# Optimization experiments

Measured on AMD Instinct MI355X. Metric: run time of the kernel, lower is better.

Reference implementation:

```python
import jax, jax.numpy as jnp
import numpy as np

P = 16      # patch size
DM = 512    # d_model
DI = 1024   # d_inner = expand * d_model
N = 16      # d_state
K = 4       # d_conv
DR = 32     # dt_rank = ceil(d_model/16)
NL = 8      # n_layers
NC = 1000   # num_classes


def _ln(x, w, b):
    m = x.mean(-1, keepdims=True)
    v = x.var(-1, keepdims=True)
    return (x - m) * jax.lax.rsqrt(v + 1e-5) * w + b


def _fpad(x, wl, wr, ht, hb):
    # torch F.pad(x, (wl, wr, ht, hb)) with possibly negative (crop) values, NCHW
    x = jnp.pad(x, ((0, 0), (0, 0), (max(ht, 0), max(hb, 0)), (max(wl, 0), max(wr, 0))))
    return x[:, :, -min(ht, 0):x.shape[2] + min(hb, 0), -min(wl, 0):x.shape[3] + min(wr, 0)]


def _mamba(x, in_w, conv_w, conv_b, xproj_w, dt_w, dt_b, A_log, Dp, out_w):
    # standard mamba_ssm Mamba layer; weights stored (in, out)
    B, L, _ = x.shape
    xz = x @ in_w                         # (B, L, 2*DI)
    xpart, z = xz[..., :DI], xz[..., DI:]
    # depthwise causal conv1d, kernel K, padding K-1 then truncate to L
    xc = jnp.pad(xpart.transpose(0, 2, 1), ((0, 0), (0, 0), (K - 1, 0)))  # (B, DI, L+K-1)
    conv = conv_b[None, :, None] + sum(conv_w[None, :, k, None] * xc[:, :, k:k + L] for k in range(K))
    u = jax.nn.silu(conv).transpose(0, 2, 1)    # (B, L, DI)
    dbc = u @ xproj_w                           # (B, L, DR + 2N)
    dt = jax.nn.softplus(dbc[..., :DR] @ dt_w + dt_b)  # (B, L, DI)
    Bm, Cm = dbc[..., DR:DR + N], dbc[..., DR + N:]
    A = -jnp.exp(A_log)                         # (DI, N)
    dA = jnp.exp(dt[..., None] * A)             # (B, L, DI, N)
    dBu = (dt * u)[..., None] * Bm[:, :, None, :]

    def step(h, inp):
        dA_t, dBu_t, C_t = inp
        h = dA_t * h + dBu_t                    # (B, DI, N)
        return h, jnp.einsum('bdn,bn->bd', h, C_t)

    h0 = jnp.zeros((B, DI, N), x.dtype)
    _, ys = jax.lax.scan(step, h0, (dA.transpose(1, 0, 2, 3), dBu.transpose(1, 0, 2, 3), Cm.transpose(1, 0, 2)))
    y = ys.transpose(1, 0, 2) + u * Dp          # (B, L, DI)
    return (y * jax.nn.silu(z)) @ out_w         # (B, L, DM)


def reference(img, patch_ln_w, patch_ln_b, patch_w, patch_b, pos_emb, cls_tok,
              ln_w, ln_b, in_w, conv_w, conv_b, xproj_w, dt_w, dt_b, A_log, D, out_w,
              head_ln_w, head_ln_b, head_w, head_b):
    shifts = ((1, -1, 0, 0), (-1, 1, 0, 0), (0, 0, 1, -1), (0, 0, -1, 1))
    x5 = jnp.concatenate([img] + [_fpad(img, *s) for s in shifts], axis=1)  # (B, 15, H, W)
    Bn, C, H, W = x5.shape
    # 'b c (h p1) (w p2) -> b (h w) (p1 p2 c)'
    x = x5.reshape(Bn, C, H // P, P, W // P, P).transpose(0, 2, 4, 3, 5, 1).reshape(Bn, (H // P) * (W // P), P * P * C)
    x = _ln(x, patch_ln_w, patch_ln_b) @ patch_w + patch_b  # (B, n, DM)
    n = x.shape[1]
    x = jnp.concatenate([x, jnp.broadcast_to(cls_tok, (Bn, 1, DM))], axis=1)  # cls appended at END
    x = x + pos_emb[:, :n + 1]
    for i in range(NL):
        y = _ln(x, ln_w[i], ln_b[i])
        x = x + _mamba(y, in_w[i], conv_w[i], conv_b[i], xproj_w[i], dt_w[i], dt_b[i], A_log[i], D[i], out_w[i])
    x = x[:, -1]  # pool='cls' -> last token
    return _ln(x, head_ln_w, head_ln_b) @ head_w + head_b


def setup_inputs() -> dict:
    key = jax.random.key(0)
    ks = jax.random.split(key, 12)
    B = 8
    PD = P * P * 15  # 3840
    rn = lambda k, shape, scale=1.0: jax.random.normal(k, shape, jnp.float32) * scale
    return {
        "img": rn(ks[0], (B, 3, 224, 224)),
        "patch_ln_w": jnp.ones((PD,), jnp.float32), "patch_ln_b": jnp.zeros((PD,), jnp.float32),
        "patch_w": rn(ks[1], (PD, DM), PD ** -0.5), "patch_b": jnp.zeros((DM,), jnp.float32),
        "pos_emb": rn(ks[2], (1, 197, DM), 0.02),
        "cls_tok": rn(ks[3], (1, 1, DM), 0.02),
        "ln_w": jnp.ones((NL, DM), jnp.float32), "ln_b": jnp.zeros((NL, DM), jnp.float32),
        "in_w": rn(ks[4], (NL, DM, 2 * DI), DM ** -0.5),
        "conv_w": rn(ks[5], (NL, DI, K), K ** -0.5),
        "conv_b": jnp.zeros((NL, DI), jnp.float32),
        "xproj_w": rn(ks[6], (NL, DI, DR + 2 * N), DI ** -0.5),
        "dt_w": rn(ks[7], (NL, DR, DI), DR ** -0.5),
        "dt_b": rn(ks[8], (NL, DI), 0.1) - 4.0,  # softplus -> small positive dt
        "A_log": jnp.log(jnp.broadcast_to(jnp.arange(1.0, N + 1.0, dtype=jnp.float32), (NL, DI, N))),
        "D": jnp.ones((NL, DI), jnp.float32),
        "out_w": rn(ks[9], (NL, DI, DM), DI ** -0.5),
        "head_ln_w": jnp.ones((DM,), jnp.float32), "head_ln_b": jnp.zeros((DM,), jnp.float32),
        "head_w": rn(ks[10], (DM, NC), DM ** -0.5), "head_b": jnp.zeros((NC,), jnp.float32),
    }
```

## Files before the change

kernel.cpp:

```cpp
#include <hip/hip_runtime.h>
#include <hip/hip_fp16.h>
#include <math.h>

#define BATCH   8
#define LSEQ    197
#define LPAD    200
#define NPATCH  196
#define NPTOK   (BATCH * NPATCH)
#define NTOK    (BATCH * LSEQ)
#define MPAD    1664
#define DMODEL  512
#define DINNER  1024
#define NSTATE  16
#define DRANK   32
#define NLAYER  8
#define NCLS    1000
#define PDIM    3840

typedef _Float16 f16x8 __attribute__((ext_vector_type(8)));
typedef float    f32x4 __attribute__((ext_vector_type(4)));
typedef unsigned short us8 __attribute__((ext_vector_type(8)));

__device__ __forceinline__ float f_rcp(float x) { return __builtin_amdgcn_rcpf(x); }
__device__ __forceinline__ float sp_silu(float x) { return x * f_rcp(1.0f + __expf(-x)); }
__device__ __forceinline__ float sp_softplus(float x) {
    return x > 20.0f ? x : __logf(1.0f + __expf(x));
}

#define DPP_ROW_SHR_STEP(P, NB, CTRL)                                          \
    {                                                                          \
        float t_[NB];                                                          \
        _Pragma("unroll")                                                      \
        for (int i_ = 0; i_ < NB; ++i_)                                        \
            t_[i_] = __int_as_float(__builtin_amdgcn_update_dpp(               \
                0, __float_as_int(P[i_]), CTRL, 0xF, 0xF, true));              \
        _Pragma("unroll")                                                      \
        for (int i_ = 0; i_ < NB; ++i_) P[i_] += t_[i_];                       \
    }

template <int NB>
__device__ __forceinline__ void row_sum16v(float* p) {
    DPP_ROW_SHR_STEP(p, NB, 0x111);
    DPP_ROW_SHR_STEP(p, NB, 0x112);
    DPP_ROW_SHR_STEP(p, NB, 0x114);
    DPP_ROW_SHR_STEP(p, NB, 0x118);
}

__device__ __forceinline__ void store_f16(char* __restrict__ Hb,
                                          int row, int k, int K, float v) {
    size_t byte = (size_t)row * (size_t)(K * 2) +
                  (size_t)(((unsigned)(k * 2)) ^ (unsigned)((row & 7) << 4));
    *(__half*)(Hb + byte) = __float2half_rn(v);
}

__device__ __forceinline__ void store_f16x4(char* __restrict__ Hb,
                                            int row, int k4, int K, float4 v) {
    size_t byte = (size_t)row * (size_t)(K * 2) +
                  (size_t)(((unsigned)(k4 * 2)) ^ (unsigned)((row & 7) << 4));
    *(ushort4*)(Hb + byte) = make_ushort4(
        __half_as_ushort(__float2half_rn(v.x)), __half_as_ushort(__float2half_rn(v.y)),
        __half_as_ushort(__float2half_rn(v.z)), __half_as_ushort(__float2half_rn(v.w)));
}

__device__ __forceinline__ float2 block_reduce2(float a, float b, float* lds) {
#pragma unroll
    for (int off = 32; off > 0; off >>= 1) {
        a += __shfl_down(a, off);
        b += __shfl_down(b, off);
    }
    int lane = threadIdx.x & 63, w = threadIdx.x >> 6;
    if (lane == 0) { lds[w] = a; lds[4 + w] = b; }
    __syncthreads();
    float sa = lds[0] + lds[1] + lds[2] + lds[3];
    float sb = lds[4] + lds[5] + lds[6] + lds[7];
    return make_float2(sa, sb);
}

__global__ __launch_bounds__(256) void k_patch_ln(
    const float* __restrict__ img, const float* __restrict__ lnw,
    const float* __restrict__ lnb, char* __restrict__ Xph) {
    __shared__ float vals[PDIM];
    __shared__ float red[8];
    int tok = blockIdx.x;
    int b = tok / NPATCH, p = tok % NPATCH;
    int gy = p / 14, gx = p % 14;
    int tid = threadIdx.x;
    int py = tid >> 4, px = tid & 15;
    int h0 = gy * 16 + py, w0 = gx * 16 + px;
    const int dh[5] = {0, 0, 0, -1, 1};
    const int dw[5] = {0, -1, 1, 0, 0};
    float s = 0.f, ss = 0.f;
#pragma unroll
    for (int c = 0; c < 15; ++c) {
        int g = c / 3, ch = c % 3;
        int h = h0 + dh[g], w = w0 + dw[g];
        float v = 0.f;
        if ((unsigned)h < 224u && (unsigned)w < 224u)
            v = img[((b * 3 + ch) * 224 + h) * 224 + w];
        vals[tid * 15 + c] = v;
        s += v; ss += v * v;
    }
    float2 t2 = block_reduce2(s, ss, red);
    float mean = t2.x * (1.0f / PDIM);
    float var  = t2.y * (1.0f / PDIM) - mean * mean;
    float rstd = 1.0f / sqrtf(var + 1e-5f);
    for (int j = 0; j < 15; ++j) {
        int e = tid + j * 256;
        float v = (vals[e] - mean) * rstd * lnw[e] + lnb[e];
        store_f16(Xph, tok, e, PDIM, v);
    }
}

__global__ __launch_bounds__(256) void k_ln(
    const float* __restrict__ x, const float* __restrict__ w,
    const float* __restrict__ b, char* __restrict__ yh) {
    __shared__ float red[8];
    int t = blockIdx.x, tid = threadIdx.x;
    const float* xr = x + (size_t)t * DMODEL;
    float v0 = xr[tid], v1 = xr[tid + 256];
    float2 t2 = block_reduce2(v0 + v1, v0 * v0 + v1 * v1, red);
    float mean = t2.x * (1.0f / DMODEL);
    float var  = t2.y * (1.0f / DMODEL) - mean * mean;
    float rstd = 1.0f / sqrtf(var + 1e-5f);
    store_f16(yh, t, tid,       DMODEL, (v0 - mean) * rstd * w[tid]       + b[tid]);
    store_f16(yh, t, tid + 256, DMODEL, (v1 - mean) * rstd * w[tid + 256] + b[tid + 256]);
}

__global__ __launch_bounds__(256) void k_red_ln(
    const float* __restrict__ part, float* __restrict__ xtok,
    const float* __restrict__ w, const float* __restrict__ b,
    char* __restrict__ yh) {
    __shared__ float red[8];
    int t = blockIdx.x, tid = threadIdx.x;
    size_t base = (size_t)t * DMODEL;
    float v0 = xtok[base + tid], v1 = xtok[base + tid + 256];
#pragma unroll
    for (int k = 0; k < 4; ++k) {
        v0 += part[(size_t)k * (NTOK * DMODEL) + base + tid];
        v1 += part[(size_t)k * (NTOK * DMODEL) + base + tid + 256];
    }
    xtok[base + tid] = v0;
    xtok[base + tid + 256] = v1;
    float2 t2 = block_reduce2(v0 + v1, v0 * v0 + v1 * v1, red);
    float mean = t2.x * (1.0f / DMODEL);
    float var  = t2.y * (1.0f / DMODEL) - mean * mean;
    float rstd = 1.0f / sqrtf(var + 1e-5f);
    store_f16(yh, t, tid,       DMODEL, (v0 - mean) * rstd * w[tid]       + b[tid]);
    store_f16(yh, t, tid + 256, DMODEL, (v1 - mean) * rstd * w[tid + 256] + b[tid + 256]);
}

__global__ __launch_bounds__(256) void k_wT(
    const float* __restrict__ W, char* __restrict__ Th,
    int Ks, int Ns, size_t wStride, size_t tByteStride) {
    __shared__ float t[32][33];
    int z = blockIdx.z;
    const float* Wz = W + (size_t)z * wStride;
    char* ThZ = Th + (size_t)z * tByteStride;
    int n0 = blockIdx.x * 32, k0 = blockIdx.y * 32;
    int tx = threadIdx.x, ty = threadIdx.y;
#pragma unroll
    for (int r = 0; r < 4; ++r) {
        int k = k0 + ty + r * 8, n = n0 + tx;
        t[tx][ty + r * 8] = (n < Ns) ? Wz[(size_t)k * Ns + n] : 0.f;
    }
    __syncthreads();
#pragma unroll
    for (int r = 0; r < 4; ++r) {
        int n = n0 + ty + r * 8, k = k0 + tx;
        float v = t[ty + r * 8][tx];
        size_t byte = (size_t)n * (size_t)(Ks * 2) +
                      (size_t)(((unsigned)(k * 2)) ^ (unsigned)((n & 7) << 4));
        *(__half*)(ThZ + byte) = __float2half_rn(v);
    }
}

template <bool F16OUT>
__global__ __launch_bounds__(256, 2) void k_gemm_f16(
    const char* __restrict__ Ah, const char* __restrict__ Bh,
    float* __restrict__ C, unsigned short* __restrict__ C16,
    int M, int N, int K, int kchunk, long partStride) {
    __shared__ __half L[2][2][128 * 64];
    const int tid = threadIdx.x, w = tid >> 6, lane = tid & 63;

    const int GX = gridDim.x, GY = gridDim.y;
    const int nwg = GX * GY * gridDim.z;
    const int orig = blockIdx.x + GX * (blockIdx.y + GY * blockIdx.z);
    const int q = nwg >> 3, r = nwg & 7, xcd = orig & 7, pos = orig >> 3;
    const int wrk = (xcd < r ? xcd * (q + 1) : r * (q + 1) + (xcd - r) * q) + pos;
    const int bm = wrk % GY;
    const int t1 = wrk / GY;
    const int bn = t1 % GX, bz = t1 / GX;

    const int m0 = bm * 128, n0 = bn * 128;
    const int kbeg = bz * kchunk;
    int kend = kbeg + kchunk; if (kend > K) kend = K;
    C += (size_t)bz * (size_t)partStride;
    const size_t K2 = (size_t)K * 2;
    const int srowBase = 32 * w;
    const int srLane = lane >> 3;
    const int scol = (lane & 7) * 16;

    f32x4 acc[4][4];
#pragma unroll
    for (int i = 0; i < 4; ++i)
#pragma unroll
        for (int j = 0; j < 4; ++j) acc[i][j] = (f32x4)(0.f);

    auto STAGE = [&](int buf, int k0) {
#pragma unroll
        for (int t = 0; t < 4; ++t) {
            int lr = srowBase + 8 * t;
            size_t ao = (size_t)(m0 + lr + srLane) * K2 + (size_t)k0 * 2 + scol;
            size_t bo = (size_t)(n0 + lr + srLane) * K2 + (size_t)k0 * 2 + scol;
            __builtin_amdgcn_global_load_lds(
                (const __attribute__((address_space(1))) void*)(Ah + ao),
                (__attribute__((address_space(3))) void*)&L[buf][0][lr * 64], 16, 0, 0);
            __builtin_amdgcn_global_load_lds(
                (const __attribute__((address_space(1))) void*)(Bh + bo),
                (__attribute__((address_space(3))) void*)&L[buf][1][lr * 64], 16, 0, 0);
        }
    };

    const int wr = (w >> 1) * 64, wc = (w & 1) * 64;
    const int g = lane >> 4, rr = lane & 15;
    const int nk = (kend - kbeg + 63) / 64;

    STAGE(0, kbeg);

    for (int t = 0; t < nk; ++t) {
        int cur = t & 1;
        if (t + 1 < nk) {
            STAGE(cur ^ 1, kbeg + (t + 1) * 64);
            asm volatile("s_waitcnt vmcnt(8)" ::: "memory");
        } else {
            asm volatile("s_waitcnt vmcnt(0)" ::: "memory");
        }
        __builtin_amdgcn_s_barrier();
        const __half* LA = L[cur][0];
        const __half* LB = L[cur][1];
#pragma unroll
        for (int kk = 0; kk < 2; ++kk) {
            f16x8 af[4], bf[4];
#pragma unroll
            for (int mf = 0; mf < 4; ++mf) {
                int row = wr + mf * 16 + rr;
                int off = row * 128 + ((kk * 64 + g * 16) ^ ((row & 7) << 4));
                af[mf] = *(const f16x8*)((const char*)LA + off);
            }
#pragma unroll
            for (int nf = 0; nf < 4; ++nf) {
                int row = wc + nf * 16 + rr;
                int off = row * 128 + ((kk * 64 + g * 16) ^ ((row & 7) << 4));
                bf[nf] = *(const f16x8*)((const char*)LB + off);
            }
#pragma unroll
            for (int mf = 0; mf < 4; ++mf)
#pragma unroll
                for (int nf = 0; nf < 4; ++nf)
                    acc[mf][nf] = __builtin_amdgcn_mfma_f32_16x16x32_f16(
                        af[mf], bf[nf], acc[mf][nf], 0, 0, 0);
        }
        __builtin_amdgcn_s_barrier();
    }

#pragma unroll
    for (int mf = 0; mf < 4; ++mf)
#pragma unroll
        for (int nf = 0; nf < 4; ++nf)
#pragma unroll
            for (int e = 0; e < 4; ++e) {
                int gm = m0 + wr + mf * 16 + g * 4 + e;
                int gn = n0 + wc + nf * 16 + rr;
                if (gm < M && gn < N) {
                    if (F16OUT)
                        C16[(size_t)gm * N + gn] =
                            __half_as_ushort(__float2half_rn(acc[mf][nf][e]));
                    else
                        C[(size_t)gm * N + gn] = acc[mf][nf][e];
                }
            }
}

template <int SK, bool ACC>
__global__ __launch_bounds__(256) void k_reduce(
    const float* __restrict__ part, float* __restrict__ out, int total, int stride) {
    int i = blockIdx.x * 256 + threadIdx.x;
    if (i >= total) return;
    float s = 0.f;
#pragma unroll
    for (int k = 0; k < SK; ++k) s += part[(size_t)k * stride + i];
    out[i] = ACC ? out[i] + s : s;
}

__global__ __launch_bounds__(256) void k_assemble(
    const float* __restrict__ Pe, const float* __restrict__ patch_b,
    const float* __restrict__ cls, const float* __restrict__ pos,
    float* __restrict__ xtok) {
    int idx = blockIdx.x * 256 + threadIdx.x;
    if (idx >= NTOK * DMODEL) return;
    int d = idx % DMODEL;
    int t = (idx / DMODEL) % LSEQ;
    int b = idx / (DMODEL * LSEQ);
    float v = (t < NPATCH) ? (Pe[((size_t)b * NPATCH + t) * DMODEL + d] + patch_b[d])
                           : cls[d];
    xtok[idx] = v + pos[t * DMODEL + d];
}

__global__ __launch_bounds__(256) void k_conv(
    const unsigned short* __restrict__ xzH, const float* __restrict__ cw,
    const float* __restrict__ cb, char* __restrict__ uh) {
    int idx = blockIdx.x * 256 + threadIdx.x;
    if (idx >= NTOK * (DINNER / 4)) return;
    int dq = idx & (DINNER / 4 - 1);
    int t  = idx / (DINNER / 4);
    int l  = t % LSEQ;
    int d  = dq * 4;
    float4 w0 = *(const float4*)&cw[(d + 0) * 4];
    float4 w1 = *(const float4*)&cw[(d + 1) * 4];
    float4 w2 = *(const float4*)&cw[(d + 2) * 4];
    float4 w3 = *(const float4*)&cw[(d + 3) * 4];
    float4 acc = *(const float4*)&cb[d];
#pragma unroll
    for (int j = 0; j < 4; ++j) {
        int ls = l - 3 + j;
        if (ls >= 0) {
            union { ushort4 v; __half h[4]; } xu;
            xu.v = *(const ushort4*)&xzH[(size_t)(t - 3 + j) * (2 * DINNER) + d];
            acc.x += (&w0.x)[j] * __half2float(xu.h[0]);
            acc.y += (&w1.x)[j] * __half2float(xu.h[1]);
            acc.z += (&w2.x)[j] * __half2float(xu.h[2]);
            acc.w += (&w3.x)[j] * __half2float(xu.h[3]);
        }
    }
    float4 uv = make_float4(sp_silu(acc.x), sp_silu(acc.y),
                            sp_silu(acc.z), sp_silu(acc.w));
    store_f16x4(uh, t, d, DINNER, uv);
}

__global__ __launch_bounds__(256) void k_scan2(
    const char* __restrict__ uH, const float* __restrict__ dbc,
    const float* __restrict__ dtw, const float* __restrict__ dtb,
    const float* __restrict__ Alog, const float* __restrict__ Dp,
    const unsigned short* __restrict__ xzH, char* __restrict__ gh) {
    __shared__ float uS[LPAD * 16];
    __shared__ float dS[LPAD * 16];
    __shared__ float bS[LPAD * 16];
    __shared__ float cS[LPAD * 16];
    __shared__ float wS[DRANK * 16];
    const int tid = threadIdx.x;
    const int b = blockIdx.y, d0 = blockIdx.x * 16;

    for (int i = tid; i < DRANK * 16; i += 256)
        wS[i] = dtw[(size_t)(i >> 4) * DINNER + d0 + (i & 15)];
    __syncthreads();

    for (int i = tid; i < LPAD * 2; i += 256) {
        int l = i >> 1, jj = i & 1;
        float* dst = &uS[l * 16 + jj * 8];
        if (l >= LSEQ) {
#pragma unroll
            for (int e = 0; e < 8; ++e) dst[e] = 0.f;
            continue;
        }
        int t = b * LSEQ + l;
        size_t byte = (size_t)t * (DINNER * 2) +
                      (size_t)(((unsigned)(d0 * 2 + jj * 16)) ^ (unsigned)((t & 7) << 4));
        union { us8 v; __half h[8]; } uu;
        uu.v = *(const us8*)(uH + byte);
#pragma unroll
        for (int e = 0; e < 8; ++e) dst[e] = __half2float(uu.h[e]);
    }

    const float* dbcB = dbc + ((size_t)b * LSEQ) * 64;
    for (int i = tid; i < LPAD * 4; i += 256) {
        int l = i >> 2, j = (i & 3) << 2;
        if (l >= LSEQ) {
            float4 z = make_float4(0.f, 0.f, 0.f, 0.f);
            *(float4*)&dS[l * 16 + j] = z;
            *(float4*)&bS[l * 16 + j] = z;
            *(float4*)&cS[l * 16 + j] = z;
            continue;
        }
        *(float4*)&bS[l * 16 + j] = *(const float4*)&dbcB[(size_t)l * 64 + DRANK + j];
        *(float4*)&cS[l * 16 + j] = *(const float4*)&dbcB[(size_t)l * 64 + DRANK + 16 + j];
        float4 acc = *(const float4*)&dtb[d0 + j];
#pragma unroll
        for (int kq = 0; kq < DRANK / 4; ++kq) {
            float4 r4 = *(const float4*)&dbcB[(size_t)l * 64 + kq * 4];
#pragma unroll
            for (int m = 0; m < 4; ++m) {
                float rv = (&r4.x)[m];
                float4 w4 = *(const float4*)&wS[(kq * 4 + m) * 16 + j];
                acc.x += rv * w4.x; acc.y += rv * w4.y;
                acc.z += rv * w4.z; acc.w += rv * w4.w;
            }
        }
        dS[l * 16 + j + 0] = sp_softplus(acc.x);
        dS[l * 16 + j + 1] = sp_softplus(acc.y);
        dS[l * 16 + j + 2] = sp_softplus(acc.z);
        dS[l * 16 + j + 3] = sp_softplus(acc.w);
    }
    const int n = tid & 15, dsub = tid >> 4;
    const int d = d0 + dsub;
    const float A  = -__expf(Alog[d * NSTATE + n]);
    const float Dv = Dp[d];
    __syncthreads();

    float hn = 0.f;
    float dtc[8], uvc[8], Bnc[8], Cnc[8];
#pragma unroll
    for (int i = 0; i < 8; ++i) {
        int o = i * 16;
        dtc[i] = dS[o + dsub]; uvc[i] = uS[o + dsub];
        Bnc[i] = bS[o + n];    Cnc[i] = cS[o + n];
    }
    for (int lb = 0; lb < LPAD; lb += 8) {
        float dtN[8], uvN[8], BnN[8], CnN[8];
        if (lb + 8 < LPAD) {
#pragma unroll
            for (int i = 0; i < 8; ++i) {
                int o = (lb + 8 + i) * 16;
                dtN[i] = dS[o + dsub]; uvN[i] = uS[o + dsub];
                BnN[i] = bS[o + n];    CnN[i] = cS[o + n];
            }
        } else {
#pragma unroll
            for (int i = 0; i < 8; ++i) { dtN[i] = uvN[i] = BnN[i] = CnN[i] = 0.f; }
        }
        float a8[8], b8[8], p8[8];
#pragma unroll
        for (int i = 0; i < 8; ++i) {
            a8[i] = __expf(dtc[i] * A);
            b8[i] = dtc[i] * uvc[i] * Bnc[i];
        }
#pragma unroll
        for (int i = 0; i < 8; ++i) {
            hn = a8[i] * hn + b8[i];
            p8[i] = hn * Cnc[i];
        }
        row_sum16v<8>(p8);
#pragma unroll
        for (int i = 0; i < 8; ++i)
            if (n == 15) dS[(lb + i) * 16 + dsub] = p8[i] + uvc[i] * Dv;
#pragma unroll
        for (int i = 0; i < 8; ++i) {
            dtc[i] = dtN[i]; uvc[i] = uvN[i]; Bnc[i] = BnN[i]; Cnc[i] = CnN[i];
        }
    }
    __syncthreads();

    for (int i = tid; i < LSEQ * 4; i += 256) {
        int l = i >> 2, j = (i & 3) << 2;
        int t = b * LSEQ + l;
        union { ushort4 v; __half h[4]; } zu;
        zu.v = *(const ushort4*)&xzH[(size_t)t * (2 * DINNER) + DINNER + d0 + j];
        float4 g4 = make_float4(
            dS[l * 16 + j + 0] * sp_silu(__half2float(zu.h[0])),
            dS[l * 16 + j + 1] * sp_silu(__half2float(zu.h[1])),
            dS[l * 16 + j + 2] * sp_silu(__half2float(zu.h[2])),
            dS[l * 16 + j + 3] * sp_silu(__half2float(zu.h[3])));
        store_f16x4(gh, t, d0 + j, DINNER, g4);
    }
}

__global__ __launch_bounds__(256) void k_head_ln(
    const float* __restrict__ part, const float* __restrict__ xtok,
    const float* __restrict__ lnw, const float* __restrict__ lnb,
    float* __restrict__ xr) {
    __shared__ float red[8];
    int b = blockIdx.x, tid = threadIdx.x;
    size_t base = ((size_t)(b * LSEQ + NPATCH)) * DMODEL;
    float v0 = xtok[base + tid], v1 = xtok[base + tid + 256];
#pragma unroll
    for (int k = 0; k < 4; ++k) {
        v0 += part[(size_t)k * (NTOK * DMODEL) + base + tid];
        v1 += part[(size_t)k * (NTOK * DMODEL) + base + tid + 256];
    }
    float2 t2 = block_reduce2(v0 + v1, v0 * v0 + v1 * v1, red);
    float mean = t2.x * (1.0f / DMODEL);
    float var  = t2.y * (1.0f / DMODEL) - mean * mean;
    float rstd = 1.0f / sqrtf(var + 1e-5f);
    xr[b * DMODEL + tid]       = (v0 - mean) * rstd * lnw[tid] + lnb[tid];
    xr[b * DMODEL + tid + 256] = (v1 - mean) * rstd * lnw[tid + 256] + lnb[tid + 256];
}

__global__ __launch_bounds__(256) void k_head_fc(
    const float* __restrict__ xr, const float* __restrict__ hw,
    float* __restrict__ hpart) {
    __shared__ float xs[64];
    int tid = threadIdx.x;
    int c = blockIdx.x * 256 + tid;
    int b = blockIdx.y, ks = blockIdx.z;
    if (tid < 64) xs[tid] = xr[b * DMODEL + ks * 64 + tid];
    __syncthreads();
    if (c >= NCLS) return;
    float acc = 0.f;
#pragma unroll 8
    for (int k = 0; k < 64; ++k) acc += xs[k] * hw[(size_t)(ks * 64 + k) * NCLS + c];
    hpart[(size_t)(ks * BATCH + b) * NCLS + c] = acc;
}

__global__ __launch_bounds__(256) void k_head_red(
    const float* __restrict__ hpart, const float* __restrict__ hb,
    float* __restrict__ out) {
    int i = blockIdx.x * 256 + threadIdx.x;
    if (i >= BATCH * NCLS) return;
    int b = i / NCLS, c = i % NCLS;
    float s = hb[c];
#pragma unroll
    for (int ks = 0; ks < 8; ++ks) s += hpart[(size_t)(ks * BATCH + b) * NCLS + c];
    out[i] = s;
}

extern "C" void kernel_launch(void* const* d_in, const int* in_sizes, int n_in,
                              void* d_out, int out_size, void* d_ws, size_t ws_size,
                              hipStream_t stream) {
    const float* img     = (const float*)d_in[0];
    const float* plnw    = (const float*)d_in[1];
    const float* plnb    = (const float*)d_in[2];
    const float* patch_w = (const float*)d_in[3];
    const float* patch_b = (const float*)d_in[4];
    const float* pos     = (const float*)d_in[5];
    const float* cls     = (const float*)d_in[6];
    const float* ln_w    = (const float*)d_in[7];
    const float* ln_b    = (const float*)d_in[8];
    const float* in_w    = (const float*)d_in[9];
    const float* conv_w  = (const float*)d_in[10];
    const float* conv_b  = (const float*)d_in[11];
    const float* xproj   = (const float*)d_in[12];
    const float* dt_w    = (const float*)d_in[13];
    const float* dt_b    = (const float*)d_in[14];
    const float* A_log   = (const float*)d_in[15];
    const float* Dp      = (const float*)d_in[16];
    const float* out_w   = (const float*)d_in[17];
    const float* hlnw    = (const float*)d_in[18];
    const float* hlnb    = (const float*)d_in[19];
    const float* head_w  = (const float*)d_in[20];
    const float* head_b  = (const float*)d_in[21];
    float* out = (float*)d_out;

    char* p = (char*)d_ws;
    auto alloc = [&](size_t bytes) { char* r = p; p += (bytes + 255) & ~(size_t)255; return r; };
    float* xtok = (float*)alloc((size_t)NTOK * DMODEL * 4);
    unsigned short* xzH = (unsigned short*)alloc((size_t)NTOK * 2 * DINNER * 2);
    float* dbc  = (float*)alloc((size_t)NTOK * 64 * 4);
    float* Pe   = (float*)alloc((size_t)NPTOK * DMODEL * 4);
    float* part = (float*)alloc((size_t)4 * NTOK * DMODEL * 4);
    float* xr   = (float*)alloc((size_t)BATCH * DMODEL * 4);
    float* hpart= (float*)alloc((size_t)8 * BATCH * NCLS * 4);
    char* ylnH = alloc((size_t)MPAD * DMODEL * 2);
    char* uH   = alloc((size_t)MPAD * DINNER * 2);
    char* gH   = alloc((size_t)MPAD * DINNER * 2);
    char* XpH  = alloc((size_t)MPAD * PDIM * 2);
    char* inTH  = alloc((size_t)NLAYER * 2 * DINNER * DMODEL * 2);
    char* outTH = alloc((size_t)NLAYER * DMODEL * DINNER * 2);
    char* patTH = alloc((size_t)DMODEL * PDIM * 2);
    char* xprTH = alloc((size_t)NLAYER * 128 * DINNER * 2);

    const size_t IN_T_B  = (size_t)2 * DINNER * DMODEL * 2;
    const size_t OUT_T_B = (size_t)DMODEL * DINNER * 2;
    const size_t XPR_T_B = (size_t)128 * DINNER * 2;

    k_wT<<<dim3(2 * DINNER / 32, DMODEL / 32, NLAYER), dim3(32, 8), 0, stream>>>(
        in_w, inTH, DMODEL, 2 * DINNER, (size_t)DMODEL * 2 * DINNER, IN_T_B);
    k_wT<<<dim3(DMODEL / 32, DINNER / 32, NLAYER), dim3(32, 8), 0, stream>>>(
        out_w, outTH, DINNER, DMODEL, (size_t)DINNER * DMODEL, OUT_T_B);
    k_wT<<<dim3(DMODEL / 32, PDIM / 32, 1), dim3(32, 8), 0, stream>>>(
        patch_w, patTH, PDIM, DMODEL, 0, 0);
    k_wT<<<dim3(128 / 32, DINNER / 32, NLAYER), dim3(32, 8), 0, stream>>>(
        xproj, xprTH, DINNER, 64, (size_t)DINNER * 64, XPR_T_B);

    k_patch_ln<<<NPTOK, 256, 0, stream>>>(img, plnw, plnb, XpH);
    k_gemm_f16<false><<<dim3(4, 13, 4), 256, 0, stream>>>(
        XpH, patTH, part, nullptr, NPTOK, DMODEL, PDIM, 960, (long)NPTOK * DMODEL);
    k_reduce<4, false><<<(NPTOK * DMODEL + 255) / 256, 256, 0, stream>>>(
        part, Pe, NPTOK * DMODEL, NPTOK * DMODEL);
    k_assemble<<<(NTOK * DMODEL + 255) / 256, 256, 0, stream>>>(Pe, patch_b, cls, pos, xtok);

    for (int i = 0; i < NLAYER; ++i) {
        if (i == 0) {
            k_ln<<<NTOK, 256, 0, stream>>>(xtok, ln_w, ln_b, ylnH);
        } else {
            k_red_ln<<<NTOK, 256, 0, stream>>>(part, xtok, ln_w + i * DMODEL,
                                               ln_b + i * DMODEL, ylnH);
        }
        k_gemm_f16<true><<<dim3(16, 13, 1), 256, 0, stream>>>(
            ylnH, inTH + i * IN_T_B, nullptr, xzH, NTOK, 2 * DINNER, DMODEL, DMODEL, 0);
        k_conv<<<(NTOK * (DINNER / 4) + 255) / 256, 256, 0, stream>>>(
            xzH, conv_w + (size_t)i * DINNER * 4, conv_b + (size_t)i * DINNER, uH);
        k_gemm_f16<false><<<dim3(1, 13, 8), 256, 0, stream>>>(
            uH, xprTH + i * XPR_T_B, part, nullptr, NTOK, 64, DINNER, 128, (long)NTOK * 64);
        k_reduce<8, false><<<(NTOK * 64 + 255) / 256, 256, 0, stream>>>(
            part, dbc, NTOK * 64, NTOK * 64);
        k_scan2<<<dim3(DINNER / 16, BATCH), 256, 0, stream>>>(
            uH, dbc, dt_w + (size_t)i * DRANK * DINNER, dt_b + (size_t)i * DINNER,
            A_log + (size_t)i * DINNER * NSTATE, Dp + (size_t)i * DINNER,
            xzH, gH);
        k_gemm_f16<false><<<dim3(4, 13, 4), 256, 0, stream>>>(
            gH, outTH + i * OUT_T_B, part, nullptr, NTOK, DMODEL, DINNER, 256,
            (long)NTOK * DMODEL);
    }

    k_head_ln<<<BATCH, 256, 0, stream>>>(part, xtok, hlnw, hlnb, xr);
    k_head_fc<<<dim3(4, BATCH, 8), 256, 0, stream>>>(xr, head_w, hpart);
    k_head_red<<<(BATCH * NCLS + 255) / 256, 256, 0, stream>>>(hpart, head_b, out);
}
```

Baseline: 574.4 us.

## Split selective scan into two sequence chunks with carry-in correction

Result: no change. 580.0 us (+1.0%).

```diff
diff --git a/kernel.cpp b/kernel.cpp
--- a/kernel.cpp
+++ b/kernel.cpp
@@ -4,7 +4,6 @@
 
 #define BATCH   8
 #define LSEQ    197
-#define LPAD    200
 #define NPATCH  196
 #define NPTOK   (BATCH * NPATCH)
 #define NTOK    (BATCH * LSEQ)
@@ -17,6 +16,10 @@
 #define NCLS    1000
 #define PDIM    3840
 
+#define SCL     104
+#define SLP     208
+#define LSTR    212
+
 typedef _Float16 f16x8 __attribute__((ext_vector_type(8)));
 typedef float    f32x4 __attribute__((ext_vector_type(4)));
 typedef unsigned short us8 __attribute__((ext_vector_type(8)));
@@ -60,6 +63,17 @@
     *(ushort4*)(Hb + byte) = make_ushort4(
         __half_as_ushort(__float2half_rn(v.x)), __half_as_ushort(__float2half_rn(v.y)),
         __half_as_ushort(__float2half_rn(v.z)), __half_as_ushort(__float2half_rn(v.w)));
+}
+
+__device__ __forceinline__ void store_f16x8(char* __restrict__ Hb,
+                                            int row, int k8, int K, const float* v) {
+    size_t byte = (size_t)row * (size_t)(K * 2) +
+                  (size_t)(((unsigned)(k8 * 2)) ^ (unsigned)((row & 7) << 4));
+    us8 o;
+#pragma unroll
+    for (int e = 0; e < 8; ++e)
+        o[e] = __half_as_ushort(__float2half_rn(v[e]));
+    *(us8*)(Hb + byte) = o;
 }
 
 __device__ __forceinline__ float2 block_reduce2(float a, float b, float* lds) {
@@ -337,29 +351,28 @@
     store_f16x4(uh, t, d, DINNER, uv);
 }
 
-__global__ __launch_bounds__(256) void k_scan2(
+__global__ __launch_bounds__(512) void k_scan2(
     const char* __restrict__ uH, const float* __restrict__ dbc,
     const float* __restrict__ dtw, const float* __restrict__ dtb,
     const float* __restrict__ Alog, const float* __restrict__ Dp,
     const unsigned short* __restrict__ xzH, char* __restrict__ gh) {
-    __shared__ float uS[LPAD * 16];
-    __shared__ float dS[LPAD * 16];
-    __shared__ float bS[LPAD * 16];
-    __shared__ float cS[LPAD * 16];
+    __shared__ float uS[16 * LSTR];
+    __shared__ float dS[16 * LSTR];
+    __shared__ float bS[16 * LSTR];
+    __shared__ float cS[16 * LSTR];
     __shared__ float wS[DRANK * 16];
+    __shared__ float hfin[16 * 17];
     const int tid = threadIdx.x;
     const int b = blockIdx.y, d0 = blockIdx.x * 16;
 
-    for (int i = tid; i < DRANK * 16; i += 256)
-        wS[i] = dtw[(size_t)(i >> 4) * DINNER + d0 + (i & 15)];
+    wS[tid] = dtw[(size_t)(tid >> 4) * DINNER + d0 + (tid & 15)];
     __syncthreads();
 
-    for (int i = tid; i < LPAD * 2; i += 256) {
+    for (int i = tid; i < SLP * 2; i += 512) {
         int l = i >> 1, jj = i & 1;
-        float* dst = &uS[l * 16 + jj * 8];
         if (l >= LSEQ) {
 #pragma unroll
-            for (int e = 0; e < 8; ++e) dst[e] = 0.f;
+            for (int e = 0; e < 8; ++e) uS[(jj * 8 + e) * LSTR + l] = 0.f;
             continue;
         }
         int t = b * LSEQ + l;
@@ -368,21 +381,29 @@
         union { us8 v; __half h[8]; } uu;
         uu.v = *(const us8*)(uH + byte);
 #pragma unroll
-        for (int e = 0; e < 8; ++e) dst[e] = __half2float(uu.h[e]);
+        for (int e = 0; e < 8; ++e)
+            uS[(jj * 8 + e) * LSTR + l] = __half2float(uu.h[e]);
     }
 
     const float* dbcB = dbc + ((size_t)b * LSEQ) * 64;
-    for (int i = tid; i < LPAD * 4; i += 256) {
+    for (int i = tid; i < SLP * 4; i += 512) {
         int l = i >> 2, j = (i & 3) << 2;
         if (l >= LSEQ) {
-            float4 z = make_float4(0.f, 0.f, 0.f, 0.f);
-            *(float4*)&dS[l * 16 + j] = z;
-            *(float4*)&bS[l * 16 + j] = z;
-            *(float4*)&cS[l * 16 + j] = z;
+#pragma unroll
+            for (int e = 0; e < 4; ++e) {
+                dS[(j + e) * LSTR + l] = 0.f;
+                bS[(j + e) * LSTR + l] = 0.f;
+                cS[(j + e) * LSTR + l] = 0.f;
+            }
             continue;
         }
-        *(float4*)&bS[l * 16 + j] = *(const float4*)&dbcB[(size_t)l * 64 + DRANK + j];
-        *(float4*)&cS[l * 16 + j] = *(const float4*)&dbcB[(size_t)l * 64 + DRANK + 16 + j];
+        float4 b4 = *(const float4*)&dbcB[(size_t)l * 64 + DRANK + j];
+        float4 c4 = *(const float4*)&dbcB[(size_t)l * 64 + DRANK + 16 + j];
+#pragma unroll
+        for (int e = 0; e < 4; ++e) {
+            bS[(j + e) * LSTR + l] = (&b4.x)[e];
+            cS[(j + e) * LSTR + l] = (&c4.x)[e];
+        }
         float4 acc = *(const float4*)&dtb[d0 + j];
 #pragma unroll
         for (int kq = 0; kq < DRANK / 4; ++kq) {
@@ -395,71 +416,114 @@
                 acc.z += rv * w4.z; acc.w += rv * w4.w;
             }
         }
-        dS[l * 16 + j + 0] = sp_softplus(acc.x);
-        dS[l * 16 + j + 1] = sp_softplus(acc.y);
-        dS[l * 16 + j + 2] = sp_softplus(acc.z);
-        dS[l * 16 + j + 3] = sp_softplus(acc.w);
-    }
-    const int n = tid & 15, dsub = tid >> 4;
+        dS[(j + 0) * LSTR + l] = sp_softplus(acc.x);
+        dS[(j + 1) * LSTR + l] = sp_softplus(acc.y);
+        dS[(j + 2) * LSTR + l] = sp_softplus(acc.z);
+        dS[(j + 3) * LSTR + l] = sp_softplus(acc.w);
+    }
+
+    const int c = tid >> 8;
+    const int t8 = tid & 255;
+    const int n = t8 & 15, dsub = t8 >> 4;
     const int d = d0 + dsub;
     const float A  = -__expf(Alog[d * NSTATE + n]);
     const float Dv = Dp[d];
     __syncthreads();
 
-    float hn = 0.f;
-    float dtc[8], uvc[8], Bnc[8], Cnc[8];
-#pragma unroll
-    for (int i = 0; i < 8; ++i) {
-        int o = i * 16;
-        dtc[i] = dS[o + dsub]; uvc[i] = uS[o + dsub];
-        Bnc[i] = bS[o + n];    Cnc[i] = cS[o + n];
-    }
-    for (int lb = 0; lb < LPAD; lb += 8) {
-        float dtN[8], uvN[8], BnN[8], CnN[8];
-        if (lb + 8 < LPAD) {
+    {
+        const int lbase = c * SCL;
+        float* dCol = &dS[dsub * LSTR];
+        float* uCol = &uS[dsub * LSTR];
+        float* bCol = &bS[n * LSTR];
+        float* cCol = &cS[n * LSTR];
+        float hn = 0.f, P = 1.f;
+        f32x4 dtc0 = *(f32x4*)&dCol[lbase],     dtc1 = *(f32x4*)&dCol[lbase + 4];
+        f32x4 uvc0 = *(f32x4*)&uCol[lbase],     uvc1 = *(f32x4*)&uCol[lbase + 4];
+        f32x4 Bn0  = *(f32x4*)&bCol[lbase],     Bn1  = *(f32x4*)&bCol[lbase + 4];
+        f32x4 Cn0  = *(f32x4*)&cCol[lbase],     Cn1  = *(f32x4*)&cCol[lbase + 4];
+        for (int bt = 0; bt < SCL / 8; ++bt) {
+            int lb = lbase + bt * 8;
+            f32x4 dtn0, dtn1, uvn0, uvn1, Bm0, Bm1, Cm0, Cm1;
+            if (bt + 1 < SCL / 8) {
+                int ln = lb + 8;
+                dtn0 = *(f32x4*)&dCol[ln]; dtn1 = *(f32x4*)&dCol[ln + 4];
+                uvn0 = *(f32x4*)&uCol[ln]; uvn1 = *(f32x4*)&uCol[ln + 4];
+                Bm0  = *(f32x4*)&bCol[ln]; Bm1  = *(f32x4*)&bCol[ln + 4];
+                Cm0  = *(f32x4*)&cCol[ln]; Cm1  = *(f32x4*)&cCol[ln + 4];
+            } else {
+                dtn0 = dtn1 = uvn0 = uvn1 = (f32x4)(0.f);
+                Bm0 = Bm1 = Cm0 = Cm1 = (f32x4)(0.f);
+            }
+            float dt8[8], uv8[8], B8[8], C8[8];
+#pragma unroll
+            for (int i = 0; i < 4; ++i) {
+                dt8[i] = dtc0[i]; dt8[i + 4] = dtc1[i];
+                uv8[i] = uvc0[i]; uv8[i + 4] = uvc1[i];
+                B8[i]  = Bn0[i];  B8[i + 4]  = Bn1[i];
+                C8[i]  = Cn0[i];  C8[i + 4]  = Cn1[i];
+            }
+            float a8[8], bb8[8], p8[8];
 #pragma unroll
             for (int i = 0; i < 8; ++i) {
-                int o = (lb + 8 + i) * 16;
-                dtN[i] = dS[o + dsub]; uvN[i] = uS[o + dsub];
-                BnN[i] = bS[o + n];    CnN[i] = cS[o + n];
-            }
-        } else {
-#pragma unroll
-            for (int i = 0; i < 8; ++i) { dtN[i] = uvN[i] = BnN[i] = CnN[i] = 0.f; }
-        }
-        float a8[8], b8[8], p8[8];
-#pragma unroll
-        for (int i = 0; i < 8; ++i) {
-            a8[i] = __expf(dtc[i] * A);
-            b8[i] = dtc[i] * uvc[i] * Bnc[i];
-        }
-#pragma unroll
-        for (int i = 0; i < 8; ++i) {
-            hn = a8[i] * hn + b8[i];
-            p8[i] = hn * Cnc[i];
-        }
-        row_sum16v<8>(p8);
-#pragma unroll
-        for (int i = 0; i < 8; ++i)
-            if (n == 15) dS[(lb + i) * 16 + dsub] = p8[i] + uvc[i] * Dv;
-#pragma unroll
-        for (int i = 0; i < 8; ++i) {
-            dtc[i] = dtN[i]; uvc[i] = uvN[i]; Bnc[i] = BnN[i]; Cnc[i] = CnN[i];
-        }
+                a8[i]  = __expf(dt8[i] * A);
+                bb8[i] = dt8[i] * uv8[i] * B8[i];
+            }
+#pragma unroll
+            for (int i = 0; i < 8; ++i) {
+                hn = a8[i] * hn + bb8[i];
+                p8[i] = hn * C8[i];
+            }
+            if (c == 1) {
+                float Pl[8];
+#pragma unroll
+                for (int i = 0; i < 8; ++i) { P *= a8[i]; Pl[i] = P; }
+                if (dsub == 0) {
+#pragma unroll
+                    for (int i = 0; i < 8; ++i) cCol[lb + i] = C8[i] * Pl[i];
+                }
+            }
+            row_sum16v<8>(p8);
+            if (n == 15) {
+#pragma unroll
+                for (int i = 0; i < 8; ++i) dCol[lb + i] = p8[i] + uv8[i] * Dv;
+            }
+            dtc0 = dtn0; dtc1 = dtn1; uvc0 = uvn0; uvc1 = uvn1;
+            Bn0 = Bm0; Bn1 = Bm1; Cn0 = Cm0; Cn1 = Cm1;
+        }
+        if (c == 0) hfin[dsub * 17 + n] = hn;
     }
     __syncthreads();
 
-    for (int i = tid; i < LSEQ * 4; i += 256) {
-        int l = i >> 2, j = (i & 3) << 2;
+    {
+        const float h0 = hfin[dsub * 17 + n];
+        float* dCol = &dS[dsub * LSTR];
+        const float* cCol = &cS[n * LSTR];
+        const int lstart = SCL + c * (SCL / 2);
+        for (int bt = 0; bt < SCL / 8; ++bt) {
+            int lc = lstart + bt * 4;
+            f32x4 cp = *(f32x4*)&cCol[lc];
+            float p4[4];
+#pragma unroll
+            for (int i = 0; i < 4; ++i) p4[i] = cp[i] * h0;
+            row_sum16v<4>(p4);
+            if (n == 15) {
+#pragma unroll
+                for (int i = 0; i < 4; ++i) dCol[lc + i] += p4[i];
+            }
+        }
+    }
+    __syncthreads();
+
+    for (int i = tid; i < LSEQ * 2; i += 512) {
+        int l = i >> 1, jj = i & 1;
         int t = b * LSEQ + l;
-        union { ushort4 v; __half h[4]; } zu;
-        zu.v = *(const ushort4*)&xzH[(size_t)t * (2 * DINNER) + DINNER + d0 + j];
-        float4 g4 = make_float4(
-            dS[l * 16 + j + 0] * sp_silu(__half2float(zu.h[0])),
-            dS[l * 16 + j + 1] * sp_silu(__half2float(zu.h[1])),
-            dS[l * 16 + j + 2] * sp_silu(__half2float(zu.h[2])),
-            dS[l * 16 + j + 3] * sp_silu(__half2float(zu.h[3])));
-        store_f16x4(gh, t, d0 + j, DINNER, g4);
+        union { us8 v; __half h[8]; } zu;
+        zu.v = *(const us8*)&xzH[(size_t)t * (2 * DINNER) + DINNER + d0 + jj * 8];
+        float g8[8];
+#pragma unroll
+        for (int e = 0; e < 8; ++e)
+            g8[e] = dS[(jj * 8 + e) * LSTR + l] * sp_silu(__half2float(zu.h[e]));
+        store_f16x8(gh, t, d0 + jj * 8, DINNER, g8);
     }
 }
 
@@ -592,7 +656,7 @@
             uH, xprTH + i * XPR_T_B, part, nullptr, NTOK, 64, DINNER, 128, (long)NTOK * 64);
         k_reduce<8, false><<<(NTOK * 64 + 255) / 256, 256, 0, stream>>>(
             part, dbc, NTOK * 64, NTOK * 64);
-        k_scan2<<<dim3(DINNER / 16, BATCH), 256, 0, stream>>>(
+        k_scan2<<<dim3(DINNER / 16, BATCH), 512, 0, stream>>>(
             uH, dbc, dt_w + (size_t)i * DRANK * DINNER, dt_b + (size_t)i * DINNER,
             A_log + (size_t)i * DINNER * NSTATE, Dp + (size_t)i * DINNER,
             xzH, gH);
```
